# Performance work log

Measured on AMD Instinct MI355X. Metric: run time of the kernel, lower is better.

## Reference

```python
import jax, jax.numpy as jnp
import numpy as np

K = 3                      # kernel size
PAD = 1
GAIN = 1.4142135623730951  # torch calculate_gain('relu') = sqrt(2)
STD_SPATIAL = GAIN / K     # FilterNorm spatial, running_std=False -> scalar
EPS = 1e-10
NEG_SLOPE = 0.1
RES_SCALE = 1.0


def _filter_norm_spatial(f):
    # f: [B, K*K, H, W]; normalize across the K*K filter channels per pixel
    m = f.mean(axis=1, keepdims=True)
    s = f.std(axis=1, keepdims=True, ddof=1)  # torch std is unbiased
    return (f - m) / (s + EPS) * STD_SPATIAL


def _filter_norm_channel(f, std_ch, C):
    # f: [B, C*K*K]; normalize over the K*K taps of each channel
    B = f.shape[0]
    f = f.reshape(B, C, K * K)
    m = f.mean(axis=2, keepdims=True)
    s = f.std(axis=2, keepdims=True, ddof=1)
    f = (f - m) / (s + EPS)
    return f.reshape(B, -1) * std_ch  # learned per-element std (running_std=True)


def _ddf_mul(x, cf, sf):
    # x: [B,C,H,W], cf: [B,C,K*K], sf: [B,K*K,H,W]
    # out[b,c,i,j] = sum_t x_pad[b,c,i+u(t),j+v(t)] * cf[b,c,t] * sf[b,t,i,j]
    B, C, H, W = x.shape
    xp = jnp.pad(x, ((0, 0), (0, 0), (PAD, PAD), (PAD, PAD)))
    out = jnp.zeros_like(x)
    for t in range(K * K):  # small fixed loop over 9 taps
        u, v = t // K, t % K
        patch = xp[:, :, u:u + H, v:v + W]
        out = out + patch * cf[:, :, t, None, None] * sf[:, t:t + 1, :, :]
    return out


def _ddfpack(x, Ws, bs, W1, b1, W2, b2, std_ch):
    B, C, H, W = x.shape
    # spatial branch: 1x1 conv C -> K*K, then FilterNorm('spatial')
    sf = jnp.einsum('bchw,kc->bkhw', x, Ws) + bs[None, :, None, None]
    sf = _filter_norm_spatial(sf)
    # channel branch: GAP -> fc -> relu -> fc -> FilterNorm('channel')
    pooled = x.mean(axis=(2, 3))                       # [B, C]
    h = jax.nn.relu(pooled @ W1.T + b1)                # [B, mid]
    cf = h @ W2.T + b2                                 # [B, C*K*K]
    cf = _filter_norm_channel(cf, std_ch, C).reshape(B, C, K * K)
    return _ddf_mul(x, cf, sf)


def setup_inputs() -> dict:
    key = jax.random.key(0)
    ks = jax.random.split(key, 10)
    B, C, H, W = 16, 64, 192, 192
    mid = int(C * 0.2)  # se_ratio = 0.2 -> 12
    return {
        'x': jax.random.normal(ks[0], (B, C, H, W), jnp.float32),
        'Ws': jax.random.normal(ks[1], (K * K, C), jnp.float32) * 0.1,
        'bs': jax.random.normal(ks[2], (K * K,), jnp.float32) * 0.1,
        'W1': jax.random.normal(ks[3], (mid, C), jnp.float32) * 0.1,
        'b1': jax.random.normal(ks[4], (mid,), jnp.float32) * 0.1,
        'W2': jax.random.normal(ks[5], (C * K * K, mid), jnp.float32) * 0.1,
        'b2': jax.random.normal(ks[6], (C * K * K,), jnp.float32) * 0.1,
        'std_ch': jax.random.normal(ks[7], (C * K * K,), jnp.float32) * STD_SPATIAL,
        'Wc': jax.random.normal(ks[8], (C, C, K, K), jnp.float32) * 0.05,
        'bc': jax.random.normal(ks[9], (C,), jnp.float32) * 0.05,
    }


def reference(x, Ws, bs, W1, b1, W2, b2, std_ch, Wc, bc):
    out = _ddfpack(x, Ws, bs, W1, b1, W2, b2, std_ch)
    out = jnp.where(out >= 0, out, NEG_SLOPE * out)  # LeakyReLU(0.1)
    out = jax.lax.conv_general_dilated(
        out, Wc, window_strides=(1, 1), padding='SAME',
        dimension_numbers=('NCHW', 'OIHW', 'NCHW'))
    out = out + bc[None, :, None, None]
    return x + out * RES_SCALE
```

## Files before the change

kernel.cpp:

```cpp
#include <hip/hip_runtime.h>

typedef unsigned short ushort_t;
typedef unsigned int uint_t;

typedef __attribute__((ext_vector_type(8))) __bf16 bf16x8;
typedef __attribute__((ext_vector_type(4))) float f32x4;

#define HH 192
#define WW 192
#define HWD (192*192)
#define CC 64
#define BB 16

__device__ __forceinline__ float b2f(uint_t u) {
    return __uint_as_float((u & 0xffffu) << 16);
}
__device__ __forceinline__ ushort_t f2b(float f) {
    uint_t x = __float_as_uint(f);
    uint_t r = x + 0x7fffu + ((x >> 16) & 1u);
    return (ushort_t)(r >> 16);
}
__device__ __forceinline__ bf16x8 zero8() {
    uint4 z; z.x = 0; z.y = 0; z.z = 0; z.w = 0;
    return __builtin_bit_cast(bf16x8, z);
}
__device__ __forceinline__ bf16x8 ld8(const ushort_t* p) {
    return __builtin_bit_cast(bf16x8, *(const uint4*)p);
}

__global__ void k_prep(const float* __restrict__ Wc, ushort_t* __restrict__ wt) {
    int i = blockIdx.x * 256 + threadIdx.x;
    if (i < 9 * 64 * 64) {
        int t  = i >> 12;
        int co = (i >> 6) & 63;
        int ci = i & 63;
        wt[i] = f2b(Wc[(co * 64 + ci) * 9 + t]);
    }
}

__global__ void k_pool(const float* __restrict__ x, float* __restrict__ pooled) {
    int c = blockIdx.x, b = blockIdx.y, tid = threadIdx.x;
    const float4* xp = (const float4*)(x + (size_t)(b * 64 + c) * HWD);
    float s = 0.f;
    for (int i = tid; i < HWD / 4; i += 256) {
        float4 u = xp[i];
        s += u.x + u.y + u.z + u.w;
    }
    __shared__ float red[4];
    for (int o = 32; o > 0; o >>= 1) s += __shfl_down(s, o, 64);
    if ((tid & 63) == 0) red[tid >> 6] = s;
    __syncthreads();
    if (tid == 0) pooled[b * 64 + c] = (red[0] + red[1] + red[2] + red[3]) * (1.f / (float)HWD);
}

__global__ void k_mlp(const float* __restrict__ pooled,
                      const float* __restrict__ W1, const float* __restrict__ b1,
                      const float* __restrict__ W2, const float* __restrict__ b2,
                      const float* __restrict__ std_ch, float* __restrict__ cf) {
    int b = blockIdx.x, tid = threadIdx.x;
    __shared__ float pl[64], hv[12];
    pl[tid] = pooled[b * 64 + tid];
    __syncthreads();
    if (tid < 12) {
        float h = b1[tid];
        for (int c = 0; c < 64; c++) h += pl[c] * W1[tid * 64 + c];
        hv[tid] = h > 0.f ? h : 0.f;
    }
    __syncthreads();
    int c = tid;
    float r[9]; float m = 0.f;
    #pragma unroll
    for (int t = 0; t < 9; t++) {
        float v = b2[c * 9 + t];
        #pragma unroll
        for (int k = 0; k < 12; k++) v += hv[k] * W2[(c * 9 + t) * 12 + k];
        r[t] = v; m += v;
    }
    m *= (1.f / 9.f);
    float var = 0.f;
    #pragma unroll
    for (int t = 0; t < 9; t++) { float d = r[t] - m; var += d * d; }
    var *= (1.f / 8.f);
    float inv = 1.f / (sqrtf(var) + 1e-10f);
    #pragma unroll
    for (int t = 0; t < 9; t++)
        cf[(b * 64 + c) * 9 + t] = (r[t] - m) * inv * std_ch[c * 9 + t];
}

__global__ __launch_bounds__(256, 2)
void k_fused(const float* __restrict__ x, const float* __restrict__ Ws,
             const float* __restrict__ bs, const float* __restrict__ cf,
             ushort_t* __restrict__ y) {
    __shared__ ushort_t xt[64 * 434];
    __shared__ float sfL[256 * 12];
    __shared__ float WsL[576];
    __shared__ float cfL[576];
    __shared__ float bsL[9];

    int b = blockIdx.y;
    int tw = blockIdx.x % 3, th = blockIdx.x / 3;
    int h0 = th * 4, w0 = tw * 64;
    int tid = threadIdx.x;

    for (int i = tid; i < 576; i += 256) { WsL[i] = Ws[i]; cfL[i] = cf[b * 576 + i]; }
    if (tid < 9) bsL[tid] = bs[tid];

    const float* xb = x + (size_t)b * 64 * HWD;
    #pragma unroll
    for (int j = 0; j < 27; j++) {
        int idx = tid + j * 256;
        int c = idx / 108;
        int rem = idx - c * 108;
        int r = rem / 18, seg = rem - r * 18;
        int gr = h0 - 1 + r;
        int gw0 = w0 - 4 + seg * 4;
        float4 v;
        if (gr >= 0 && gr < HH && gw0 >= 0 && gw0 < WW)
            v = *(const float4*)(xb + (size_t)c * HWD + (size_t)gr * WW + gw0);
        else { v.x = 0.f; v.y = 0.f; v.z = 0.f; v.w = 0.f; }
        int o = c * 434 + r * 72 + seg * 4;
        *(uint_t*)(&xt[o])     = (uint_t)f2b(v.x) | ((uint_t)f2b(v.y) << 16);
        *(uint_t*)(&xt[o + 2]) = (uint_t)f2b(v.z) | ((uint_t)f2b(v.w) << 16);
    }
    __syncthreads();

    {
        int hl = tid >> 6, wl = tid & 63;
        float s[9];
        #pragma unroll
        for (int t = 0; t < 9; t++) s[t] = bsL[t];
        int base = (hl + 1) * 72 + wl + 4;
        for (int c = 0; c < 64; c++) {
            float xv = b2f(xt[c * 434 + base]);
            #pragma unroll
            for (int t = 0; t < 9; t++) s[t] += xv * WsL[t * 64 + c];
        }
        float m = 0.f;
        #pragma unroll
        for (int t = 0; t < 9; t++) m += s[t];
        m *= (1.f / 9.f);
        float var = 0.f;
        #pragma unroll
        for (int t = 0; t < 9; t++) { float d = s[t] - m; var += d * d; }
        var *= (1.f / 8.f);
        float inv = 0.4714045207910317f / (sqrtf(var) + 1e-10f);
        #pragma unroll
        for (int t = 0; t < 9; t++) sfL[tid * 12 + t] = (s[t] - m) * inv;
    }
    __syncthreads();

    int lane = tid & 63;
    int hl = tid >> 6;
    float cfv[9];
    #pragma unroll
    for (int t = 0; t < 9; t++) cfv[t] = cfL[lane * 9 + t];
    const uint_t* lds32 = (const uint_t*)xt;
    int gh = h0 + hl;
    size_t yrow = ((size_t)b * HWD + (size_t)gh * WW + w0) * 64 + lane;

    for (int k = 0; k < 64; k++) {
        const f32x4* sp = (const f32x4*)&sfL[(hl * 64 + k) * 12];
        f32x4 s0 = sp[0], s1 = sp[1];
        float s8 = sfL[(hl * 64 + k) * 12 + 8];
        float wv[9];
        wv[0] = cfv[0] * s0[0]; wv[1] = cfv[1] * s0[1]; wv[2] = cfv[2] * s0[2];
        wv[3] = cfv[3] * s0[3]; wv[4] = cfv[4] * s1[0]; wv[5] = cfv[5] * s1[1];
        wv[6] = cfv[6] * s1[2]; wv[7] = cfv[7] * s1[3]; wv[8] = cfv[8] * s8;

        int p0 = k + 3;
        int a = p0 & ~1;
        bool odd = (p0 & 1) != 0;
        float acc = 0.f;
        #pragma unroll
        for (int r = 0; r < 3; r++) {
            int di = lane * 217 + (hl + r) * 36 + (a >> 1);
            uint_t d0 = lds32[di], d1 = lds32[di + 1];
            float v0 = b2f(d0), v1 = b2f(d0 >> 16), v2 = b2f(d1), v3 = b2f(d1 >> 16);
            float xa = odd ? v1 : v0;
            float xm = odd ? v2 : v1;
            float xc = odd ? v3 : v2;
            acc += xa * wv[r * 3 + 0] + xm * wv[r * 3 + 1] + xc * wv[r * 3 + 2];
        }
        float v = acc >= 0.f ? acc : 0.1f * acc;
        y[yrow + (size_t)k * 64] = f2b(v);
    }
}

__global__ __launch_bounds__(256, 2)
void k_conv(const ushort_t* __restrict__ y, const ushort_t* __restrict__ wt,
            const float* __restrict__ x, const float* __restrict__ bc,
            float* __restrict__ out) {
    int tid = threadIdx.x;
    int lane = tid & 63, ln = lane & 15, quad = lane >> 4;
    int wid = blockIdx.x * 4 + (tid >> 6);
    int phi = wid & 1;
    int g0 = wid >> 1;

    bf16x8 wf[9][2][2];
    #pragma unroll
    for (int t = 0; t < 9; t++)
        #pragma unroll
        for (int ks = 0; ks < 2; ks++)
            #pragma unroll
            for (int mt = 0; mt < 2; mt++) {
                int co = phi * 32 + mt * 16 + ln;
                wf[t][ks][mt] = ld8(wt + ((t * 64 + co) * 64 + ks * 32 + quad * 8));
            }
    float bcv[2][4];
    #pragma unroll
    for (int mt = 0; mt < 2; mt++)
        #pragma unroll
        for (int r = 0; r < 4; r++)
            bcv[mt][r] = bc[phi * 32 + mt * 16 + quad * 4 + r];

    for (int g = g0; g < BB * HH * (WW / 16); g += 2048) {
        int b = g / (HH * (WW / 16));
        int rem = g - b * (HH * (WW / 16));
        int h = rem / (WW / 16);
        int w0 = (rem % (WW / 16)) * 16;
        f32x4 acc[2];
        #pragma unroll
        for (int mt = 0; mt < 2; mt++) {
            acc[mt][0] = bcv[mt][0]; acc[mt][1] = bcv[mt][1];
            acc[mt][2] = bcv[mt][2]; acc[mt][3] = bcv[mt][3];
        }
        const ushort_t* yb = y + (size_t)b * HWD * 64;
        #pragma unroll
        for (int t = 0; t < 9; t++) {
            const int u_ = t / 3, v_ = t % 3;
            int sh = h + u_ - 1;
            int sw = w0 + ln + v_ - 1;
            bool ok = (sh >= 0) & (sh < HH) & (sw >= 0) & (sw < WW);
            #pragma unroll
            for (int ks = 0; ks < 2; ks++) {
                bf16x8 bfr;
                if (ok) bfr = ld8(yb + (size_t)(sh * WW + sw) * 64 + ks * 32 + quad * 8);
                else    bfr = zero8();
                acc[0] = __builtin_amdgcn_mfma_f32_16x16x32_bf16(wf[t][ks][0], bfr, acc[0], 0, 0, 0);
                acc[1] = __builtin_amdgcn_mfma_f32_16x16x32_bf16(wf[t][ks][1], bfr, acc[1], 0, 0, 0);
            }
        }
        #pragma unroll
        for (int mt = 0; mt < 2; mt++)
            #pragma unroll
            for (int r = 0; r < 4; r++) {
                int co = phi * 32 + mt * 16 + quad * 4 + r;
                size_t off = (size_t)(b * 64 + co) * HWD + h * WW + w0 + ln;
                out[off] = acc[mt][r] + x[off];
            }
    }
}

extern "C" void kernel_launch(void* const* d_in, const int* in_sizes, int n_in,
                              void* d_out, int out_size, void* d_ws, size_t ws_size,
                              hipStream_t stream) {
    const float* x      = (const float*)d_in[0];
    const float* Ws     = (const float*)d_in[1];
    const float* bs     = (const float*)d_in[2];
    const float* W1     = (const float*)d_in[3];
    const float* b1     = (const float*)d_in[4];
    const float* W2     = (const float*)d_in[5];
    const float* b2     = (const float*)d_in[6];
    const float* std_ch = (const float*)d_in[7];
    const float* Wc     = (const float*)d_in[8];
    const float* bc     = (const float*)d_in[9];
    float* out = (float*)d_out;

    char* ws = (char*)d_ws;
    float*    pooled = (float*)(ws);
    float*    cf     = (float*)(ws + 4096);
    ushort_t* wt     = (ushort_t*)(ws + 40960);
    ushort_t* y      = (ushort_t*)(ws + 131072);

    k_prep<<<dim3(144), dim3(256), 0, stream>>>(Wc, wt);
    k_pool<<<dim3(64, 16), dim3(256), 0, stream>>>(x, pooled);
    k_mlp<<<dim3(16), dim3(64), 0, stream>>>(pooled, W1, b1, W2, b2, std_ch, cf);
    k_fused<<<dim3(144, 16), dim3(256), 0, stream>>>(x, Ws, bs, cf, y);
    k_conv<<<dim3(1024), dim3(256), 0, stream>>>(y, wt, x, bc, out);
}
```

Before: 611.4 us.

## Stage conv input halo tiles in swizzled LDS and reuse across taps

The 3x3 conv kernel now assigns each block a 4x64 output tile and cooperatively loads a 6x66 halo tile of the bf16 intermediate into LDS, using an XOR swizzle to avoid bank conflicts. All nine MFMA taps read from LDS instead of issuing repeated global loads with bounds checks. The residual x values are prefetched before the MFMA chain, and the block ids are remapped to improve locality. This trades about 50KB of LDS per block, which may limit occupancy, and a blocking sync before compute for less global/L2 traffic.

```diff
diff --git a/kernel.cpp b/kernel.cpp
--- a/kernel.cpp
+++ b/kernel.cpp
@@ -186,15 +186,43 @@
     }
 }
 
+#define CONV_LDS_BYTES (6 * 66 * 128)
+
 __global__ __launch_bounds__(256, 2)
 void k_conv(const ushort_t* __restrict__ y, const ushort_t* __restrict__ wt,
             const float* __restrict__ x, const float* __restrict__ bc,
             float* __restrict__ out) {
+    __shared__ char yt[CONV_LDS_BYTES];
+
+    int bid = blockIdx.x;
+    int swz = (bid & 7) * 288 + (bid >> 3);
+    int b = swz / 144;
+    int rem = swz - b * 144;
+    int ht = rem / 3;
+    int wtile = rem - ht * 3;
+    int h0 = ht * 4, w0 = wtile * 64;
+
     int tid = threadIdx.x;
     int lane = tid & 63, ln = lane & 15, quad = lane >> 4;
-    int wid = blockIdx.x * 4 + (tid >> 6);
-    int phi = wid & 1;
-    int g0 = wid >> 1;
+    int wv_ = tid >> 6, phi = wv_ & 1, rr = wv_ >> 1;
+
+    const ushort_t* yb = y + (size_t)b * HWD * 64;
+    #pragma unroll
+    for (int j = 0; j < 13; j++) {
+        int i = tid + j * 256;
+        if (i < 6 * 66 * 8) {
+            int row = i / 528;
+            int r2 = i - row * 528;
+            int p = r2 >> 3, c = r2 & 7;
+            int gh = h0 - 1 + row, gw = w0 - 1 + p;
+            uint4 v;
+            if (gh >= 0 && gh < HH && gw >= 0 && gw < WW)
+                v = *(const uint4*)(yb + ((size_t)(gh * WW + gw) * 64 + c * 8));
+            else { v.x = 0; v.y = 0; v.z = 0; v.w = 0; }
+            int off = ((row * 66 + p) << 7) + ((c ^ (p & 7)) << 4);
+            *(uint4*)(yt + off) = v;
+        }
+    }
 
     bf16x8 wf[9][2][2];
     #pragma unroll
@@ -213,41 +241,49 @@
         for (int r = 0; r < 4; r++)
             bcv[mt][r] = bc[phi * 32 + mt * 16 + quad * 4 + r];
 
-    for (int g = g0; g < BB * HH * (WW / 16); g += 2048) {
-        int b = g / (HH * (WW / 16));
-        int rem = g - b * (HH * (WW / 16));
-        int h = rem / (WW / 16);
-        int w0 = (rem % (WW / 16)) * 16;
-        f32x4 acc[2];
-        #pragma unroll
-        for (int mt = 0; mt < 2; mt++) {
-            acc[mt][0] = bcv[mt][0]; acc[mt][1] = bcv[mt][1];
-            acc[mt][2] = bcv[mt][2]; acc[mt][3] = bcv[mt][3];
+    __syncthreads();
+
+    for (int orr = 0; orr < 2; orr++) {
+        int orow = rr * 2 + orr;
+        int gh = h0 + orow;
+        #pragma unroll
+        for (int s = 0; s < 4; s++) {
+            size_t o0 = (size_t)(b * 64 + phi * 32) * HWD + (size_t)gh * WW + w0 + s * 16 + ln;
+            float xv[2][4];
+            #pragma unroll
+            for (int mt = 0; mt < 2; mt++)
+                #pragma unroll
+                for (int r = 0; r < 4; r++)
+                    xv[mt][r] = x[o0 + (size_t)(mt * 16 + quad * 4 + r) * HWD];
+
+            f32x4 acc[2];
+            #pragma unroll
+            for (int mt = 0; mt < 2; mt++) {
+                acc[mt][0] = bcv[mt][0]; acc[mt][1] = bcv[mt][1];
+                acc[mt][2] = bcv[mt][2]; acc[mt][3] = bcv[mt][3];
+            }
+
+            #pragma unroll
+            for (int t = 0; t < 9; t++) {
+                const int u_ = t / 3, v_ = t % 3;
+                int p = s * 16 + ln + v_;
+                int boff = ((orow + u_) * 66 + p) << 7;
+                int a0 = boff + ((quad ^ (p & 7)) << 4);
+                int a1 = a0 ^ 64;
+                bf16x8 f0 = __builtin_bit_cast(bf16x8, *(const uint4*)(yt + a0));
+                bf16x8 f1 = __builtin_bit_cast(bf16x8, *(const uint4*)(yt + a1));
+                acc[0] = __builtin_amdgcn_mfma_f32_16x16x32_bf16(wf[t][0][0], f0, acc[0], 0, 0, 0);
+                acc[1] = __builtin_amdgcn_mfma_f32_16x16x32_bf16(wf[t][0][1], f0, acc[1], 0, 0, 0);
+                acc[0] = __builtin_amdgcn_mfma_f32_16x16x32_bf16(wf[t][1][0], f1, acc[0], 0, 0, 0);
+                acc[1] = __builtin_amdgcn_mfma_f32_16x16x32_bf16(wf[t][1][1], f1, acc[1], 0, 0, 0);
+            }
+
+            #pragma unroll
+            for (int mt = 0; mt < 2; mt++)
+                #pragma unroll
+                for (int r = 0; r < 4; r++)
+                    out[o0 + (size_t)(mt * 16 + quad * 4 + r) * HWD] = acc[mt][r] + xv[mt][r];
         }
-        const ushort_t* yb = y + (size_t)b * HWD * 64;
-        #pragma unroll
-        for (int t = 0; t < 9; t++) {
-            const int u_ = t / 3, v_ = t % 3;
-            int sh = h + u_ - 1;
-            int sw = w0 + ln + v_ - 1;
-            bool ok = (sh >= 0) & (sh < HH) & (sw >= 0) & (sw < WW);
-            #pragma unroll
-            for (int ks = 0; ks < 2; ks++) {
-                bf16x8 bfr;
-                if (ok) bfr = ld8(yb + (size_t)(sh * WW + sw) * 64 + ks * 32 + quad * 8);
-                else    bfr = zero8();
-                acc[0] = __builtin_amdgcn_mfma_f32_16x16x32_bf16(wf[t][ks][0], bfr, acc[0], 0, 0, 0);
-                acc[1] = __builtin_amdgcn_mfma_f32_16x16x32_bf16(wf[t][ks][1], bfr, acc[1], 0, 0, 0);
-            }
-        }
-        #pragma unroll
-        for (int mt = 0; mt < 2; mt++)
-            #pragma unroll
-            for (int r = 0; r < 4; r++) {
-                int co = phi * 32 + mt * 16 + quad * 4 + r;
-                size_t off = (size_t)(b * 64 + co) * HWD + h * WW + w0 + ln;
-                out[off] = acc[mt][r] + x[off];
-            }
     }
 }
 
@@ -276,5 +312,5 @@
     k_pool<<<dim3(64, 16), dim3(256), 0, stream>>>(x, pooled);
     k_mlp<<<dim3(16), dim3(64), 0, stream>>>(pooled, W1, b1, W2, b2, std_ch, cf);
     k_fused<<<dim3(144, 16), dim3(256), 0, stream>>>(x, Ws, bs, cf, y);
-    k_conv<<<dim3(1024), dim3(256), 0, stream>>>(y, wt, x, bc, out);
-}
+    k_conv<<<dim3(2304), dim3(256), 0, stream>>>(y, wt, x, bc, out);
+}
```

Measured after the change: 513.3 us. 1.19x faster.
